# Optimization experiments

Hardware: AMD Instinct MI355X
Metric: run time of the kernel (lower is better)

Reference implementation:

```python
import jax, jax.numpy as jnp
import numpy as np

N, E, IN, H, D, G = 1024, 16384, 1300, 16, 512, 8
SLOPE = 0.2  # PyG GATConv default negative_slope


def gat_conv(x, src, dst, W, a_src, a_dst, b):
    """PyG GATConv (concat heads): per-edge score, segment softmax over dst, scatter-add."""
    n = x.shape[0]
    h = (x @ W).reshape(n, H, D)                       # [N,H,D]
    s_src = jnp.einsum('nhd,hd->nh', h, a_src)         # [N,H]
    s_dst = jnp.einsum('nhd,hd->nh', h, a_dst)
    e = jax.nn.leaky_relu(s_src[src] + s_dst[dst], SLOPE)   # [E,H]
    m = jax.ops.segment_max(e, dst, num_segments=n)
    p = jnp.exp(e - m[dst])
    alpha = p / jax.ops.segment_sum(p, dst, num_segments=n)[dst]
    out = jax.ops.segment_sum(alpha[:, :, None] * h[src], dst, num_segments=n)  # [N,H,D]
    return out.reshape(n, H * D) + b


def setup_inputs() -> dict:
    key = jax.random.key(0)
    ks = jax.random.split(key, 12)
    s = 0.05
    return {
        'x': jax.random.normal(ks[0], (N, IN), jnp.float32),
        'edge_index': jax.random.randint(ks[1], (2, E), 0, N),
        'batch': jnp.sort(jax.random.randint(ks[2], (N,), 0, G)),
        'W1': jax.random.normal(ks[3], (IN, H * D), jnp.float32) * s,
        'att_src1': jax.random.normal(ks[4], (H, D), jnp.float32) * s,
        'att_dst1': jax.random.normal(ks[5], (H, D), jnp.float32) * s,
        'b1': jnp.zeros((H * D,), jnp.float32),
        'W2': jax.random.normal(ks[6], (H * D, H * D), jnp.float32) * s,
        'att_src2': jax.random.normal(ks[7], (H, D), jnp.float32) * s,
        'att_dst2': jax.random.normal(ks[8], (H, D), jnp.float32) * s,
        'b2': jnp.zeros((H * D,), jnp.float32),
        'lin_w': jax.random.normal(ks[9], (H * D, 1), jnp.float32) * s,
        'lin_b': jnp.zeros((1,), jnp.float32),
    }


def reference(x, edge_index, batch, W1, att_src1, att_dst1, b1,
              W2, att_src2, att_dst2, b2, lin_w, lin_b):
    loops = jnp.arange(N, dtype=edge_index.dtype)      # add_self_loops=True
    src = jnp.concatenate([edge_index[0], loops])
    dst = jnp.concatenate([edge_index[1], loops])
    h = jax.nn.relu(gat_conv(x, src, dst, W1, att_src1, att_dst1, b1))
    h = jax.nn.relu(gat_conv(h, src, dst, W2, att_src2, att_dst2, b2))
    counts = jax.ops.segment_sum(jnp.ones((N,), h.dtype), batch, num_segments=G)
    pooled = jax.ops.segment_sum(h, batch, num_segments=G) / jnp.clip(counts, 1.0)[:, None]
    return (pooled @ lin_w + lin_b).squeeze(-1)        # [G]
```

## Files before the change

### kernel.cpp

```cpp
#include <hip/hip_runtime.h>


#define NN      1024
#define EE      16384
#define IN_DIM  1300
#define NH      16
#define HD      512
#define FD      8192
#define NG      8
#define ET      (EE + NN)
#define SLOPE   0.2f

typedef __attribute__((ext_vector_type(8))) short short8;
typedef __attribute__((ext_vector_type(4))) float f32x4;


__global__ void k_init_counts(int* counts) {
    int i = blockIdx.x * 256 + threadIdx.x;
    if (i < NN) counts[i] = 1;
}

__global__ void k_count(const int* __restrict__ dst, int* counts) {
    int e = blockIdx.x * 256 + threadIdx.x;
    if (e < EE) atomicAdd(&counts[dst[e]], 1);
}

__global__ void k_scan(const int* __restrict__ counts, int* __restrict__ off,
                       int* __restrict__ cursor) {
    __shared__ int s[NN];
    int t = threadIdx.x;
    s[t] = counts[t];
    __syncthreads();
    for (int d = 1; d < NN; d <<= 1) {
        int v = (t >= d) ? s[t - d] : 0;
        __syncthreads();
        s[t] += v;
        __syncthreads();
    }
    off[t + 1] = s[t];
    if (t == 0) off[0] = 0;
    cursor[t] = 0;
}

__global__ void k_fill(const int* __restrict__ srcv, const int* __restrict__ dstv,
                       const int* __restrict__ off, int* cursor, int* __restrict__ csr) {
    int e = blockIdx.x * 256 + threadIdx.x;
    if (e < EE) {
        int d = dstv[e];
        int p = atomicAdd(&cursor[d], 1);
        csr[off[d] + p] = srcv[e];
    } else if (e < ET) {
        int n = e - EE;
        int p = atomicAdd(&cursor[n], 1);
        csr[off[n] + p] = n;
    }
}


__device__ __forceinline__ int swz2(int r) {
    return (((r >> 1) & 3) ^ ((r >> 4) & 3)) << 3;
}
__device__ __forceinline__ int swz(int r) {
    return ((r & 3) ^ ((r >> 4) & 3)) << 3;
}

__device__ __forceinline__ unsigned short bf16_rne(float f) {
    unsigned int u = __float_as_uint(f);
    u += 0x7FFF + ((u >> 16) & 1);
    return (unsigned short)(u >> 16);
}

__device__ __forceinline__ void split2(float f, unsigned short& h, unsigned short& l) {
    unsigned short hh = bf16_rne(f);
    float hf = __uint_as_float(((unsigned int)hh) << 16);
    h = hh;
    l = bf16_rne(f - hf);
}


__global__ __launch_bounds__(256) void k_conv_a(const float* __restrict__ S,
                                                unsigned short* __restrict__ H,
                                                unsigned short* __restrict__ L,
                                                int K, int KT) {
    const int chunk = blockIdx.x;
    const int mt = chunk / KT, kt = chunk - mt * KT;
    const int tid = threadIdx.x;
    const size_t ob = (size_t)chunk * 4096;
#pragma unroll
    for (int half = 0; half < 2; half++) {
        const int r = (tid >> 2) + half * 64;
        const int kc0 = (tid & 3) << 3;
        const int k = kt * 32 + (kc0 ^ swz2(r));
        const float* src = S + (size_t)(mt * 128 + r) * K + k;
        float4 f0 = make_float4(0.f, 0.f, 0.f, 0.f), f1 = f0;
        if (k < K)     f0 = *(const float4*)src;
        if (k + 4 < K) f1 = *(const float4*)(src + 4);
        float vals[8] = {f0.x, f0.y, f0.z, f0.w, f1.x, f1.y, f1.z, f1.w};
        short8 hv, lv;
#pragma unroll
        for (int j = 0; j < 8; j++) {
            unsigned short h, l;
            split2(vals[j], h, l);
            hv[j] = (short)h;
            lv[j] = (short)l;
        }
        *(short8*)(H + ob + r * 32 + kc0) = hv;
        *(short8*)(L + ob + r * 32 + kc0) = lv;
    }
}

__global__ __launch_bounds__(256) void k_conv_b(const float* __restrict__ S,
                                                unsigned short* __restrict__ H,
                                                unsigned short* __restrict__ L,
                                                int K, int Nn, int KT) {
    __shared__ float T[128][33];
    const int chunk = blockIdx.x;
    const int nt = chunk / KT, kt = chunk - nt * KT;
    const int tid = threadIdx.x;
    {
        const int kr = tid >> 3;
        const int c0 = (tid & 7) << 4;
        const int k = kt * 32 + kr;
        const float* row = S + (size_t)k * Nn + nt * 128 + c0;
#pragma unroll
        for (int j = 0; j < 4; j++) {
            float4 v = (k < K) ? *(const float4*)(row + (j << 2))
                               : make_float4(0.f, 0.f, 0.f, 0.f);
            T[c0 + (j << 2) + 0][kr] = v.x;
            T[c0 + (j << 2) + 1][kr] = v.y;
            T[c0 + (j << 2) + 2][kr] = v.z;
            T[c0 + (j << 2) + 3][kr] = v.w;
        }
    }
    __syncthreads();
    const size_t ob = (size_t)chunk * 4096;
#pragma unroll
    for (int half = 0; half < 2; half++) {
        const int n = (tid >> 2) + half * 64;
        const int kc0 = (tid & 3) << 3;
        const int ks = kc0 ^ swz2(n);
        short8 hv, lv;
#pragma unroll
        for (int j = 0; j < 8; j++) {
            unsigned short h, l;
            split2(T[n][ks + j], h, l);
            hv[j] = (short)h;
            lv[j] = (short)l;
        }
        *(short8*)(H + ob + n * 32 + kc0) = hv;
        *(short8*)(L + ob + n * 32 + kc0) = lv;
    }
}


__global__ __launch_bounds__(256, 2) void k_gemm_planes(
        const unsigned short* __restrict__ Ahp, const unsigned short* __restrict__ Alp,
        const unsigned short* __restrict__ Bhp, const unsigned short* __restrict__ Blp,
        float* __restrict__ C, int KT, int Nn) {
    __shared__ short smem[4][4096];
    const int tid = threadIdx.x;
    const int lane = tid & 63;
    const int wid = tid >> 6;
    const int wr = wid >> 1, wc = wid & 1;
    const int l15 = lane & 15, l4 = lane >> 4;

    const size_t aoff = (size_t)blockIdx.y * KT * 4096;
    const size_t boff = (size_t)blockIdx.x * KT * 4096;

    f32x4 acc[4][4];
#pragma unroll
    for (int i = 0; i < 4; i++)
#pragma unroll
        for (int j = 0; j < 4; j++) acc[i][j] = (f32x4){0.f, 0.f, 0.f, 0.f};

    short8 st[4][2];
    {
        const size_t ab = aoff + tid * 8, bb = boff + tid * 8;
#pragma unroll
        for (int p = 0; p < 2; p++) {
            st[0][p] = *(const short8*)(Ahp + ab + p * 2048);
            st[1][p] = *(const short8*)(Alp + ab + p * 2048);
            st[2][p] = *(const short8*)(Bhp + bb + p * 2048);
            st[3][p] = *(const short8*)(Blp + bb + p * 2048);
        }
    }

    for (int t = 0; t < KT; t++) {
        __syncthreads();
#pragma unroll
        for (int pl = 0; pl < 4; pl++)
#pragma unroll
            for (int p = 0; p < 2; p++)
                *(short8*)&smem[pl][p * 2048 + tid * 8] = st[pl][p];

        if (t + 1 < KT) {
            const size_t ab = aoff + (size_t)(t + 1) * 4096 + tid * 8;
            const size_t bb = boff + (size_t)(t + 1) * 4096 + tid * 8;
#pragma unroll
            for (int p = 0; p < 2; p++) {
                st[0][p] = *(const short8*)(Ahp + ab + p * 2048);
                st[1][p] = *(const short8*)(Alp + ab + p * 2048);
                st[2][p] = *(const short8*)(Bhp + bb + p * 2048);
                st[3][p] = *(const short8*)(Blp + bb + p * 2048);
            }
        }
        __syncthreads();

        short8 ahf[4], alf[4];
#pragma unroll
        for (int i = 0; i < 4; i++) {
            int m = wr * 64 + i * 16 + l15;
            int ks = (l4 << 3) ^ swz2(m);
            ahf[i] = *(const short8*)&smem[0][m * 32 + ks];
            alf[i] = *(const short8*)&smem[1][m * 32 + ks];
        }
#pragma unroll
        for (int j = 0; j < 4; j++) {
            int n = wc * 64 + j * 16 + l15;
            int ks = (l4 << 3) ^ swz2(n);
            short8 bhf = *(const short8*)&smem[2][n * 32 + ks];
            short8 blf = *(const short8*)&smem[3][n * 32 + ks];
#pragma unroll
            for (int i = 0; i < 4; i++) {
                acc[i][j] = __builtin_amdgcn_mfma_f32_16x16x32_bf16(ahf[i], bhf, acc[i][j], 0, 0, 0);
                acc[i][j] = __builtin_amdgcn_mfma_f32_16x16x32_bf16(ahf[i], blf, acc[i][j], 0, 0, 0);
                acc[i][j] = __builtin_amdgcn_mfma_f32_16x16x32_bf16(alf[i], bhf, acc[i][j], 0, 0, 0);
            }
        }
    }

    float* Cp = C + (size_t)(blockIdx.y * 128 + wr * 64 + (l4 << 2)) * Nn
                  + blockIdx.x * 128 + wc * 64 + l15;
#pragma unroll
    for (int i = 0; i < 4; i++) {
#pragma unroll
        for (int r = 0; r < 4; r++) {
            float* rowp = Cp + (size_t)(i * 16 + r) * Nn;
#pragma unroll
            for (int j = 0; j < 4; j++)
                rowp[j * 16] = acc[i][j][r];
        }
    }
}


__global__ __launch_bounds__(256, 2) void k_gemm_mfma(const float* __restrict__ A,
                                                      const float* __restrict__ B,
                                                      float* __restrict__ C,
                                                      int M, int K, int Nn) {
    __shared__ unsigned short Ah[128][32];
    __shared__ unsigned short Al[128][32];
    __shared__ unsigned short Bh[128][32];
    __shared__ unsigned short Bl[128][32];

    const int tid = threadIdx.x;
    const int lane = tid & 63;
    const int wid = tid >> 6;
    const int wr = wid >> 1, wc = wid & 1;
    const int l15 = lane & 15, l4 = lane >> 4;

    const int a_r  = tid >> 1;
    const int a_k0 = (tid & 1) << 4;
    const int b_k  = tid >> 3;
    const int b_n0 = (tid & 7) << 4;

    const float* Ap = A + (size_t)(blockIdx.y * 128 + a_r) * K;
    const float* Bp = B + (size_t)blockIdx.x * 128 + b_n0;

    f32x4 acc[4][4];
#pragma unroll
    for (int i = 0; i < 4; i++)
#pragma unroll
        for (int j = 0; j < 4; j++) acc[i][j] = (f32x4){0.f, 0.f, 0.f, 0.f};

    const int nt = (K + 31) >> 5;
    const float4 z4 = make_float4(0.f, 0.f, 0.f, 0.f);

    float4 areg[4], breg[4];
    {
#pragma unroll
        for (int j = 0; j < 4; j++) {
            int k = a_k0 + (j << 2);
            areg[j] = (k < K) ? *(const float4*)(Ap + k) : z4;
        }
        bool bok = b_k < K;
#pragma unroll
        for (int j = 0; j < 4; j++)
            breg[j] = bok ? *(const float4*)(Bp + (size_t)b_k * Nn + (j << 2)) : z4;
    }

    for (int t = 0; t < nt; t++) {
        __syncthreads();
#pragma unroll
        for (int j = 0; j < 4; j++) {
            int kk = a_k0 + (j << 2);
            int ks = kk ^ swz(a_r);
            ushort4 h, l;
            split2(areg[j].x, h.x, l.x);
            split2(areg[j].y, h.y, l.y);
            split2(areg[j].z, h.z, l.z);
            split2(areg[j].w, h.w, l.w);
            *(ushort4*)&Ah[a_r][ks] = h;
            *(ushort4*)&Al[a_r][ks] = l;
        }
#pragma unroll
        for (int j = 0; j < 4; j++) {
            const float* bf = (const float*)&breg[j];
#pragma unroll
            for (int c = 0; c < 4; c++) {
                int n = b_n0 + (j << 2) + c;
                unsigned short h, l;
                split2(bf[c], h, l);
                int ks = b_k ^ swz(n);
                Bh[n][ks] = h;
                Bl[n][ks] = l;
            }
        }

        if (t + 1 < nt) {
            const int k0 = (t + 1) << 5;
#pragma unroll
            for (int j = 0; j < 4; j++) {
                int k = k0 + a_k0 + (j << 2);
                areg[j] = (k < K) ? *(const float4*)(Ap + k) : z4;
            }
            bool bok = (k0 + b_k) < K;
#pragma unroll
            for (int j = 0; j < 4; j++)
                breg[j] = bok ? *(const float4*)(Bp + (size_t)(k0 + b_k) * Nn + (j << 2)) : z4;
        }

        __syncthreads();

        short8 ahf[4], alf[4];
#pragma unroll
        for (int i = 0; i < 4; i++) {
            int m = wr * 64 + i * 16 + l15;
            int ks = (l4 << 3) ^ swz(m);
            ahf[i] = *(const short8*)&Ah[m][ks];
            alf[i] = *(const short8*)&Al[m][ks];
        }
#pragma unroll
        for (int j = 0; j < 4; j++) {
            int n = wc * 64 + j * 16 + l15;
            int ks = (l4 << 3) ^ swz(n);
            short8 bhf = *(const short8*)&Bh[n][ks];
            short8 blf = *(const short8*)&Bl[n][ks];
#pragma unroll
            for (int i = 0; i < 4; i++) {
                acc[i][j] = __builtin_amdgcn_mfma_f32_16x16x32_bf16(ahf[i], bhf, acc[i][j], 0, 0, 0);
                acc[i][j] = __builtin_amdgcn_mfma_f32_16x16x32_bf16(ahf[i], blf, acc[i][j], 0, 0, 0);
                acc[i][j] = __builtin_amdgcn_mfma_f32_16x16x32_bf16(alf[i], bhf, acc[i][j], 0, 0, 0);
            }
        }
    }

    float* Cp = C + (size_t)(blockIdx.y * 128 + wr * 64 + (l4 << 2)) * Nn
                  + blockIdx.x * 128 + wc * 64 + l15;
#pragma unroll
    for (int i = 0; i < 4; i++) {
#pragma unroll
        for (int r = 0; r < 4; r++) {
            float* rowp = Cp + (size_t)(i * 16 + r) * Nn;
#pragma unroll
            for (int j = 0; j < 4; j++)
                rowp[j * 16] = acc[i][j][r];
        }
    }
}


__global__ __launch_bounds__(256) void k_scores(const float* __restrict__ h,
                                                const float* __restrict__ a_src,
                                                const float* __restrict__ a_dst,
                                                float* __restrict__ s_src,
                                                float* __restrict__ s_dst) {
    int wid = (blockIdx.x * 256 + threadIdx.x) >> 6;
    int lane = threadIdx.x & 63;
    if (wid >= NN * NH) return;
    int n = wid >> 4, hh = wid & 15;
    const float* hp = h + (size_t)n * FD + hh * HD;
    const float* as = a_src + hh * HD;
    const float* ad = a_dst + hh * HD;
    float ss = 0.f, sd = 0.f;
    for (int d = lane; d < HD; d += 64) {
        float v = hp[d];
        ss += v * as[d];
        sd += v * ad[d];
    }
#pragma unroll
    for (int o = 32; o > 0; o >>= 1) {
        ss += __shfl_xor(ss, o);
        sd += __shfl_xor(sd, o);
    }
    if (lane == 0) { s_src[wid] = ss; s_dst[wid] = sd; }
}


#define MAXCH 64

__global__ __launch_bounds__(256) void k_attn(const float* __restrict__ h,
                                              const float* __restrict__ s_src,
                                              const float* __restrict__ s_dst,
                                              const int* __restrict__ off,
                                              const int* __restrict__ csr,
                                              const float* __restrict__ bias,
                                              float* __restrict__ out) {
    const int t = blockIdx.x;
    const int tid = threadIdx.x;
    __shared__ float m_sh[NH], den_sh[NH];
    __shared__ float alpha[MAXCH][NH];
    __shared__ int src_sh[MAXCH];

    const int e0 = off[t], e1 = off[t + 1];

    if (tid < NH) {
        int hh = tid;
        float sd = s_dst[t * NH + hh];
        float m = -3.0e38f;
        for (int e = e0; e < e1; e++) {
            float v = s_src[csr[e] * NH + hh] + sd;
            v = v > 0.f ? v : SLOPE * v;
            m = fmaxf(m, v);
        }
        float den = 0.f;
        for (int e = e0; e < e1; e++) {
            float v = s_src[csr[e] * NH + hh] + sd;
            v = v > 0.f ? v : SLOPE * v;
            den += __expf(v - m);
        }
        m_sh[hh] = m;
        den_sh[hh] = den;
    }
    __syncthreads();

    float acc[32];
#pragma unroll
    for (int j = 0; j < 32; j++) acc[j] = 0.f;

    for (int c0 = e0; c0 < e1; c0 += MAXCH) {
        int ch = min(MAXCH, e1 - c0);
        for (int i = tid; i < ch * NH; i += 256) {
            int e = i >> 4, hh = i & 15;
            int s = csr[c0 + e];
            if (hh == 0) src_sh[e] = s;
            float v = s_src[s * NH + hh] + s_dst[t * NH + hh];
            v = v > 0.f ? v : SLOPE * v;
            alpha[e][hh] = __expf(v - m_sh[hh]) / den_sh[hh];
        }
        __syncthreads();
        for (int e = 0; e < ch; e++) {
            const float* hp = h + (size_t)src_sh[e] * FD;
#pragma unroll
            for (int j = 0; j < 32; j++)
                acc[j] += alpha[e][j >> 1] * hp[tid + (j << 8)];
        }
        __syncthreads();
    }

#pragma unroll
    for (int j = 0; j < 32; j++) {
        int f = tid + (j << 8);
        float v = acc[j] + bias[f];
        out[(size_t)t * FD + f] = v > 0.f ? v : 0.f;
    }
}


__global__ __launch_bounds__(256) void k_pool(const float* __restrict__ h,
                                              const int* __restrict__ batch,
                                              float* __restrict__ pooled) {
    __shared__ int b_sh[NN];
    const int tid = threadIdx.x;
    const int f = blockIdx.x * 256 + tid;
    for (int i = tid; i < NN; i += 256) b_sh[i] = batch[i];
    __syncthreads();
    float acc[NG];
    int cnt[NG];
#pragma unroll
    for (int g = 0; g < NG; g++) { acc[g] = 0.f; cnt[g] = 0; }
    for (int n = 0; n < NN; n++) {
        int bg = b_sh[n];
        float v = h[(size_t)n * FD + f];
#pragma unroll
        for (int g = 0; g < NG; g++) {
            acc[g] += (bg == g) ? v : 0.f;
            cnt[g] += (bg == g) ? 1 : 0;
        }
    }
#pragma unroll
    for (int g = 0; g < NG; g++)
        pooled[(size_t)g * FD + f] = acc[g] / fmaxf((float)cnt[g], 1.f);
}

__global__ __launch_bounds__(256) void k_final(const float* __restrict__ pooled,
                                               const float* __restrict__ lin_w,
                                               const float* __restrict__ lin_b,
                                               float* __restrict__ outv) {
    const int g = blockIdx.x;
    const int tid = threadIdx.x;
    float s = 0.f;
    for (int f = tid; f < FD; f += 256)
        s += pooled[(size_t)g * FD + f] * lin_w[f];
    __shared__ float red[256];
    red[tid] = s;
    __syncthreads();
    for (int o = 128; o > 0; o >>= 1) {
        if (tid < o) red[tid] += red[tid + o];
        __syncthreads();
    }
    if (tid == 0) outv[g] = red[0] + lin_b[0];
}


extern "C" void kernel_launch(void* const* d_in, const int* in_sizes, int n_in,
                              void* d_out, int out_size, void* d_ws, size_t ws_size,
                              hipStream_t stream) {
    const float* x   = (const float*)d_in[0];
    const int*   ei  = (const int*)d_in[1];
    const int*   bat = (const int*)d_in[2];
    const float* W1  = (const float*)d_in[3];
    const float* as1 = (const float*)d_in[4];
    const float* ad1 = (const float*)d_in[5];
    const float* b1  = (const float*)d_in[6];
    const float* W2  = (const float*)d_in[7];
    const float* as2 = (const float*)d_in[8];
    const float* ad2 = (const float*)d_in[9];
    const float* b2  = (const float*)d_in[10];
    const float* lw  = (const float*)d_in[11];
    const float* lb  = (const float*)d_in[12];

    char* p0 = (char*)d_ws;
    char* p = p0;
    auto alloc = [&](size_t bytes) {
        char* r = p;
        p += (bytes + 255) & ~size_t(255);
        return r;
    };
    int* counts   = (int*)alloc((NN + 1) * sizeof(int));
    int* off      = (int*)alloc((NN + 1) * sizeof(int));
    int* cursor   = (int*)alloc(NN * sizeof(int));
    int* csr      = (int*)alloc(ET * sizeof(int));
    float* ssrc   = (float*)alloc((size_t)NN * NH * sizeof(float));
    float* sdst   = (float*)alloc((size_t)NN * NH * sizeof(float));
    float* hbuf   = (float*)alloc((size_t)NN * FD * sizeof(float));
    float* abuf   = (float*)alloc((size_t)NN * FD * sizeof(float));
    float* pooled = (float*)alloc((size_t)NG * FD * sizeof(float));

    const int KT1 = (IN_DIM + 31) / 32;
    const int KT2 = FD / 32;
    const size_t sz_xp  = (size_t)(NN / 128) * KT1 * 4096;
    const size_t sz_w1p = (size_t)(FD / 128) * KT1 * 4096;
    const size_t sz_w2p = (size_t)(FD / 128) * KT2 * 4096;
    const size_t sz_h2p = (size_t)(NN / 128) * KT2 * 4096;
    unsigned short* xH  = (unsigned short*)alloc(sz_xp * 2);
    unsigned short* xL  = (unsigned short*)alloc(sz_xp * 2);
    unsigned short* w1H = (unsigned short*)alloc(sz_w1p * 2);
    unsigned short* w1L = (unsigned short*)alloc(sz_w1p * 2);
    unsigned short* w2H = (unsigned short*)alloc(sz_w2p * 2);
    unsigned short* w2L = (unsigned short*)alloc(sz_w2p * 2);
    unsigned short* h2H = (unsigned short*)alloc(sz_h2p * 2);
    unsigned short* h2L = (unsigned short*)alloc(sz_h2p * 2);
    const bool planes_ok = (size_t)(p - p0) <= ws_size;

    const int* esrc = ei;
    const int* edst = ei + EE;

    k_init_counts<<<(NN + 255) / 256, 256, 0, stream>>>(counts);
    k_count<<<(EE + 255) / 256, 256, 0, stream>>>(edst, counts);
    k_scan<<<1, NN, 0, stream>>>(counts, off, cursor);
    k_fill<<<(ET + 255) / 256, 256, 0, stream>>>(esrc, edst, off, cursor, csr);

    dim3 gg(FD / 128, NN / 128);

    if (planes_ok) {
        k_conv_a<<<(NN / 128) * KT1, 256, 0, stream>>>(x, xH, xL, IN_DIM, KT1);
        k_conv_b<<<(FD / 128) * KT1, 256, 0, stream>>>(W1, w1H, w1L, IN_DIM, FD, KT1);
        k_conv_b<<<(FD / 128) * KT2, 256, 0, stream>>>(W2, w2H, w2L, FD, FD, KT2);
        k_gemm_planes<<<gg, 256, 0, stream>>>(xH, xL, w1H, w1L, hbuf, KT1, FD);
    } else {
        k_gemm_mfma<<<gg, 256, 0, stream>>>(x, W1, hbuf, NN, IN_DIM, FD);
    }
    k_scores<<<NN * NH / 4, 256, 0, stream>>>(hbuf, as1, ad1, ssrc, sdst);
    k_attn<<<NN, 256, 0, stream>>>(hbuf, ssrc, sdst, off, csr, b1, abuf);

    if (planes_ok) {
        k_conv_a<<<(NN / 128) * KT2, 256, 0, stream>>>(abuf, h2H, h2L, FD, KT2);
        k_gemm_planes<<<gg, 256, 0, stream>>>(h2H, h2L, w2H, w2L, hbuf, KT2, FD);
    } else {
        k_gemm_mfma<<<gg, 256, 0, stream>>>(abuf, W2, hbuf, NN, FD, FD);
    }
    k_scores<<<NN * NH / 4, 256, 0, stream>>>(hbuf, as2, ad2, ssrc, sdst);
    k_attn<<<NN, 256, 0, stream>>>(hbuf, ssrc, sdst, off, csr, b2, abuf);

    k_pool<<<FD / 256, 256, 0, stream>>>(abuf, bat, pooled);
    k_final<<<NG, 256, 0, stream>>>(pooled, lw, lb, (float*)d_out);
}
```

Before: 1.394 ms.

## Recast sparse attention aggregation as dense per-head attention-matrix GEMM

Replaces the gather-based k_attn aggregation with a dense path. Softmax stats are computed per destination node, the normalized edge weights are scattered into a dense [H,N,N] matrix, and that matrix is split into bf16 hi/lo planes. A per-head GEMM against the transposed h planes then does the aggregation, with bias and ReLU fused into its epilogue. The planes GEMM also switches to double-buffered direct global-to-LDS loads. The cost is a 64MB matrix that must be zeroed and converted, doing dense work on a graph with about 1.6% density.

```diff
diff --git a/kernel.cpp b/kernel.cpp
--- a/kernel.cpp
+++ b/kernel.cpp
@@ -42,6 +42,23 @@
     cursor[t] = 0;
 }
 
+__global__ void k_fill2(const int* __restrict__ srcv, const int* __restrict__ dstv,
+                        const int* __restrict__ off, int* cursor,
+                        int* __restrict__ csr, int* __restrict__ csr_dst) {
+    int e = blockIdx.x * 256 + threadIdx.x;
+    if (e < EE) {
+        int d = dstv[e];
+        int p = atomicAdd(&cursor[d], 1);
+        csr[off[d] + p] = srcv[e];
+        csr_dst[off[d] + p] = d;
+    } else if (e < ET) {
+        int n = e - EE;
+        int p = atomicAdd(&cursor[n], 1);
+        csr[off[n] + p] = n;
+        csr_dst[off[n] + p] = n;
+    }
+}
+
 __global__ void k_fill(const int* __restrict__ srcv, const int* __restrict__ dstv,
                        const int* __restrict__ off, int* cursor, int* __restrict__ csr) {
     int e = blockIdx.x * 256 + threadIdx.x;
@@ -75,6 +92,12 @@
     float hf = __uint_as_float(((unsigned int)hh) << 16);
     h = hh;
     l = bf16_rne(f - hf);
+}
+
+__device__ __forceinline__ void gload16(const void* g, void* l) {
+    __builtin_amdgcn_global_load_lds((const __attribute__((address_space(1))) void*)g,
+                                     (__attribute__((address_space(3))) void*)l,
+                                     16, 0, 0);
 }
 
 
@@ -152,19 +175,111 @@
     }
 }
 
+__global__ __launch_bounds__(256) void k_conv_pa(const float* __restrict__ Pf,
+                                                 unsigned short* __restrict__ H,
+                                                 unsigned short* __restrict__ L) {
+    const int chunk = blockIdx.x;
+    const int head = chunk >> 8;
+    const int rem = chunk & 255;
+    const int mt = rem >> 5, kt = rem & 31;
+    const int tid = threadIdx.x;
+    const size_t ob = (size_t)chunk * 4096;
+    const float* base = Pf + (size_t)head * NN * NN;
+#pragma unroll
+    for (int half = 0; half < 2; half++) {
+        const int r = (tid >> 2) + half * 64;
+        const int kc0 = (tid & 3) << 3;
+        const int k = kt * 32 + (kc0 ^ swz2(r));
+        const float* src = base + (size_t)(mt * 128 + r) * NN + k;
+        float4 f0 = *(const float4*)src;
+        float4 f1 = *(const float4*)(src + 4);
+        float vals[8] = {f0.x, f0.y, f0.z, f0.w, f1.x, f1.y, f1.z, f1.w};
+        short8 hv, lv;
+#pragma unroll
+        for (int j = 0; j < 8; j++) {
+            unsigned short h, l;
+            split2(vals[j], h, l);
+            hv[j] = (short)h;
+            lv[j] = (short)l;
+        }
+        *(short8*)(H + ob + r * 32 + kc0) = hv;
+        *(short8*)(L + ob + r * 32 + kc0) = lv;
+    }
+}
+
+
+__global__ __launch_bounds__(256) void k_stats(const float* __restrict__ ssrc,
+                                               const float* __restrict__ sdstv,
+                                               const int* __restrict__ off,
+                                               const int* __restrict__ csr,
+                                               float* __restrict__ md,
+                                               float* __restrict__ dn) {
+    const int t = blockIdx.x;
+    const int i = threadIdx.x;
+    const int head = i >> 4, sub = i & 15;
+    const int e0 = off[t], e1 = off[t + 1];
+    const float sd = sdstv[t * NH + head];
+    float m = -3.0e38f;
+    for (int e = e0 + sub; e < e1; e += 16) {
+        float v = ssrc[csr[e] * NH + head] + sd;
+        v = v > 0.f ? v : SLOPE * v;
+        m = fmaxf(m, v);
+    }
+#pragma unroll
+    for (int o = 8; o > 0; o >>= 1) m = fmaxf(m, __shfl_xor(m, o));
+    float den = 0.f;
+    for (int e = e0 + sub; e < e1; e += 16) {
+        float v = ssrc[csr[e] * NH + head] + sd;
+        v = v > 0.f ? v : SLOPE * v;
+        den += __expf(v - m);
+    }
+#pragma unroll
+    for (int o = 8; o > 0; o >>= 1) den += __shfl_xor(den, o);
+    if (sub == 0) { md[t * NH + head] = m; dn[t * NH + head] = den; }
+}
+
+__global__ void k_zero4(float4* __restrict__ p, int n4) {
+    int i = blockIdx.x * 256 + threadIdx.x;
+    const int stride = gridDim.x * 256;
+    const float4 z = make_float4(0.f, 0.f, 0.f, 0.f);
+    for (; i < n4; i += stride) p[i] = z;
+}
+
+__global__ __launch_bounds__(256) void k_scatter(const int* __restrict__ csr,
+                                                 const int* __restrict__ csr_dst,
+                                                 const float* __restrict__ ssrc,
+                                                 const float* __restrict__ sdstv,
+                                                 const float* __restrict__ md,
+                                                 const float* __restrict__ dn,
+                                                 float* __restrict__ Pf) {
+    const int e = blockIdx.x * 256 + threadIdx.x;
+    if (e >= ET) return;
+    const int s = csr[e], t = csr_dst[e];
+#pragma unroll
+    for (int hh = 0; hh < NH; hh++) {
+        float v = ssrc[s * NH + hh] + sdstv[t * NH + hh];
+        v = v > 0.f ? v : SLOPE * v;
+        float a = __expf(v - md[t * NH + hh]) / dn[t * NH + hh];
+        atomicAdd(&Pf[(size_t)hh * NN * NN + (size_t)t * NN + s], a);
+    }
+}
+
 
 __global__ __launch_bounds__(256, 2) void k_gemm_planes(
         const unsigned short* __restrict__ Ahp, const unsigned short* __restrict__ Alp,
         const unsigned short* __restrict__ Bhp, const unsigned short* __restrict__ Blp,
-        float* __restrict__ C, int KT, int Nn) {
-    __shared__ short smem[4][4096];
+        float* __restrict__ C, int KT, int Nn,
+        const float* __restrict__ bias, int relu, int headed) {
+    __shared__ short smem[2][4][4096];
     const int tid = threadIdx.x;
     const int lane = tid & 63;
     const int wid = tid >> 6;
     const int wr = wid >> 1, wc = wid & 1;
     const int l15 = lane & 15, l4 = lane >> 4;
 
-    const size_t aoff = (size_t)blockIdx.y * KT * 4096;
+    const size_t amt = headed ? ((size_t)(blockIdx.x >> 2) * 8 + blockIdx.y)
+                              : (size_t)blockIdx.y;
+    const size_t aoff = amt * KT * 4096;
     const size_t boff = (size_t)blockIdx.x * KT * 4096;
 
     f32x4 acc[4][4];
@@ -173,53 +288,45 @@
 #pragma unroll
         for (int j = 0; j < 4; j++) acc[i][j] = (f32x4){0.f, 0.f, 0.f, 0.f};
 
-    short8 st[4][2];
-    {
-        const size_t ab = aoff + tid * 8, bb = boff + tid * 8;
-#pragma unroll
-        for (int p = 0; p < 2; p++) {
-            st[0][p] = *(const short8*)(Ahp + ab + p * 2048);
-            st[1][p] = *(const short8*)(Alp + ab + p * 2048);
-            st[2][p] = *(const short8*)(Bhp + bb + p * 2048);
-            st[3][p] = *(const short8*)(Blp + bb + p * 2048);
-        }
-    }
-
-    for (int t = 0; t < KT; t++) {
-        __syncthreads();
-#pragma unroll
-        for (int pl = 0; pl < 4; pl++)
-#pragma unroll
-            for (int p = 0; p < 2; p++)
-                *(short8*)&smem[pl][p * 2048 + tid * 8] = st[pl][p];
-
-        if (t + 1 < KT) {
-            const size_t ab = aoff + (size_t)(t + 1) * 4096 + tid * 8;
-            const size_t bb = boff + (size_t)(t + 1) * 4096 + tid * 8;
-#pragma unroll
-            for (int p = 0; p < 2; p++) {
-                st[0][p] = *(const short8*)(Ahp + ab + p * 2048);
-                st[1][p] = *(const short8*)(Alp + ab + p * 2048);
-                st[2][p] = *(const short8*)(Bhp + bb + p * 2048);
-                st[3][p] = *(const short8*)(Blp + bb + p * 2048);
-            }
-        }
-        __syncthreads();
-
+    const int thg = (wid << 9) + (lane << 3);
+    const int ldw = (wid << 9);
+
+    auto STAGE = [&](int b, int t2) {
+        const size_t ca = aoff + (size_t)t2 * 4096;
+        const size_t cb = boff + (size_t)t2 * 4096;
+#pragma unroll
+        for (int q = 0; q < 2; q++) {
+            const int so = (q << 11) + thg;
+            const int lo = (q << 11) + ldw;
+            gload16(Ahp + ca + so, &smem[b][0][lo]);
+            gload16(Alp + ca + so, &smem[b][1][lo]);
+            gload16(Bhp + cb + so, &smem[b][2][lo]);
+            gload16(Blp + cb + so, &smem[b][3][lo]);
+        }
+    };
+
+    STAGE(0, 0);
+    STAGE(1, 1);
+    asm volatile("s_waitcnt vmcnt(8)" ::: "memory");
+    __builtin_amdgcn_sched_barrier(0);
+    __builtin_amdgcn_s_barrier();
+
+    int cur = 0;
+    for (int t = 0; t < KT; ++t) {
         short8 ahf[4], alf[4];
 #pragma unroll
         for (int i = 0; i < 4; i++) {
             int m = wr * 64 + i * 16 + l15;
             int ks = (l4 << 3) ^ swz2(m);
-            ahf[i] = *(const short8*)&smem[0][m * 32 + ks];
-            alf[i] = *(const short8*)&smem[1][m * 32 + ks];
+            ahf[i] = *(const short8*)&smem[cur][0][m * 32 + ks];
+            alf[i] = *(const short8*)&smem[cur][1][m * 32 + ks];
         }
 #pragma unroll
         for (int j = 0; j < 4; j++) {
             int n = wc * 64 + j * 16 + l15;
             int ks = (l4 << 3) ^ swz2(n);
-            short8 bhf = *(const short8*)&smem[2][n * 32 + ks];
-            short8 blf = *(const short8*)&smem[3][n * 32 + ks];
+            short8 bhf = *(const short8*)&smem[cur][2][n * 32 + ks];
+            short8 blf = *(const short8*)&smem[cur][3][n * 32 + ks];
 #pragma unroll
             for (int i = 0; i < 4; i++) {
                 acc[i][j] = __builtin_amdgcn_mfma_f32_16x16x32_bf16(ahf[i], bhf, acc[i][j], 0, 0, 0);
@@ -227,18 +334,41 @@
                 acc[i][j] = __builtin_amdgcn_mfma_f32_16x16x32_bf16(alf[i], bhf, acc[i][j], 0, 0, 0);
             }
         }
-    }
-
-    float* Cp = C + (size_t)(blockIdx.y * 128 + wr * 64 + (l4 << 2)) * Nn
-                  + blockIdx.x * 128 + wc * 64 + l15;
+
+        if (t + 1 < KT) {
+            asm volatile("s_waitcnt lgkmcnt(0)" ::: "memory");
+            __builtin_amdgcn_sched_barrier(0);
+            __builtin_amdgcn_s_barrier();
+            __builtin_amdgcn_sched_barrier(0);
+            if (t + 2 < KT) {
+                STAGE(cur, t + 2);
+                asm volatile("s_waitcnt vmcnt(8)" ::: "memory");
+            } else {
+                asm volatile("s_waitcnt vmcnt(0)" ::: "memory");
+            }
+            __builtin_amdgcn_sched_barrier(0);
+            __builtin_amdgcn_s_barrier();
+            cur ^= 1;
+        }
+    }
+
+    const int col0 = blockIdx.x * 128 + wc * 64 + l15;
+    float bj[4];
+#pragma unroll
+    for (int j = 0; j < 4; j++) bj[j] = bias ? bias[col0 + j * 16] : 0.f;
+
+    float* Cp = C + (size_t)(blockIdx.y * 128 + wr * 64 + (l4 << 2)) * Nn + col0;
 #pragma unroll
     for (int i = 0; i < 4; i++) {
 #pragma unroll
         for (int r = 0; r < 4; r++) {
             float* rowp = Cp + (size_t)(i * 16 + r) * Nn;
 #pragma unroll
-            for (int j = 0; j < 4; j++)
-                rowp[j * 16] = acc[i][j][r];
+            for (int j = 0; j < 4; j++) {
+                float v = acc[i][j][r] + bj[j];
+                if (relu) v = fmaxf(v, 0.f);
+                rowp[j * 16] = v;
+            }
         }
     }
 }
@@ -563,35 +693,75 @@
     unsigned short* h2L = (unsigned short*)alloc(sz_h2p * 2);
     const bool planes_ok = (size_t)(p - p0) <= ws_size;
 
+    const size_t sz_pp = (size_t)NH * 256 * 4096;
+    const size_t sz_hb = (size_t)(FD / 128) * 32 * 4096;
+    int*   csr_dst = (int*)alloc(ET * sizeof(int));
+    float* md      = (float*)alloc((size_t)NN * NH * sizeof(float));
+    float* dn      = (float*)alloc((size_t)NN * NH * sizeof(float));
+    unsigned short* PpH = (unsigned short*)alloc(sz_pp * 2);
+    unsigned short* PpL = (unsigned short*)alloc(sz_pp * 2);
+    char* U = alloc((size_t)NH * NN * NN * sizeof(float));
+    float* Pf = (float*)U;
+    unsigned short* HbH = (unsigned short*)U;
+    unsigned short* HbL = HbH + sz_hb;
+    const bool attn_ok = planes_ok && (size_t)(p - p0) <= ws_size;
+
     const int* esrc = ei;
     const int* edst = ei + EE;
 
     k_init_counts<<<(NN + 255) / 256, 256, 0, stream>>>(counts);
     k_count<<<(EE + 255) / 256, 256, 0, stream>>>(edst, counts);
     k_scan<<<1, NN, 0, stream>>>(counts, off, cursor);
-    k_fill<<<(ET + 255) / 256, 256, 0, stream>>>(esrc, edst, off, cursor, csr);
+    if (attn_ok)
+        k_fill2<<<(ET + 255) / 256, 256, 0, stream>>>(esrc, edst, off, cursor, csr, csr_dst);
+    else
+        k_fill<<<(ET + 255) / 256, 256, 0, stream>>>(esrc, edst, off, cursor, csr);
 
     dim3 gg(FD / 128, NN / 128);
+    dim3 ga(FD / 128, NN / 128);
+    const int nzero4 = NH * NN * NN / 4;
 
     if (planes_ok) {
         k_conv_a<<<(NN / 128) * KT1, 256, 0, stream>>>(x, xH, xL, IN_DIM, KT1);
         k_conv_b<<<(FD / 128) * KT1, 256, 0, stream>>>(W1, w1H, w1L, IN_DIM, FD, KT1);
         k_conv_b<<<(FD / 128) * KT2, 256, 0, stream>>>(W2, w2H, w2L, FD, FD, KT2);
-        k_gemm_planes<<<gg, 256, 0, stream>>>(xH, xL, w1H, w1L, hbuf, KT1, FD);
+        k_gemm_planes<<<gg, 256, 0, stream>>>(xH, xL, w1H, w1L, hbuf, KT1, FD,
+                                              nullptr, 0, 0);
     } else {
         k_gemm_mfma<<<gg, 256, 0, stream>>>(x, W1, hbuf, NN, IN_DIM, FD);
     }
     k_scores<<<NN * NH / 4, 256, 0, stream>>>(hbuf, as1, ad1, ssrc, sdst);
-    k_attn<<<NN, 256, 0, stream>>>(hbuf, ssrc, sdst, off, csr, b1, abuf);
+    if (attn_ok) {
+        k_stats<<<NN, 256, 0, stream>>>(ssrc, sdst, off, csr, md, dn);
+        k_zero4<<<2048, 256, 0, stream>>>((float4*)Pf, nzero4);
+        k_scatter<<<(ET + 255) / 256, 256, 0, stream>>>(csr, csr_dst, ssrc, sdst, md, dn, Pf);
+        k_conv_pa<<<NH * 256, 256, 0, stream>>>(Pf, PpH, PpL);
+        k_conv_b<<<(FD / 128) * 32, 256, 0, stream>>>(hbuf, HbH, HbL, NN, FD, 32);
+        k_gemm_planes<<<ga, 256, 0, stream>>>(PpH, PpL, HbH, HbL, abuf, 32, FD,
+                                              b1, 1, 1);
+    } else {
+        k_attn<<<NN, 256, 0, stream>>>(hbuf, ssrc, sdst, off, csr, b1, abuf);
+    }
 
     if (planes_ok) {
         k_conv_a<<<(NN / 128) * KT2, 256, 0, stream>>>(abuf, h2H, h2L, FD, KT2);
-        k_gemm_planes<<<gg, 256, 0, stream>>>(h2H, h2L, w2H, w2L, hbuf, KT2, FD);
+        k_gemm_planes<<<gg, 256, 0, stream>>>(h2H, h2L, w2H, w2L, hbuf, KT2, FD,
+                                              nullptr, 0, 0);
     } else {
         k_gemm_mfma<<<gg, 256, 0, stream>>>(abuf, W2, hbuf, NN, FD, FD);
     }
     k_scores<<<NN * NH / 4, 256, 0, stream>>>(hbuf, as2, ad2, ssrc, sdst);
-    k_attn<<<NN, 256, 0, stream>>>(hbuf, ssrc, sdst, off, csr, b2, abuf);
+    if (attn_ok) {
+        k_stats<<<NN, 256, 0, stream>>>(ssrc, sdst, off, csr, md, dn);
+        k_zero4<<<2048, 256, 0, stream>>>((float4*)Pf, nzero4);
+        k_scatter<<<(ET + 255) / 256, 256, 0, stream>>>(csr, csr_dst, ssrc, sdst, md, dn, Pf);
+        k_conv_pa<<<NH * 256, 256, 0, stream>>>(Pf, PpH, PpL);
+        k_conv_b<<<(FD / 128) * 32, 256, 0, stream>>>(hbuf, HbH, HbL, NN, FD, 32);
+        k_gemm_planes<<<ga, 256, 0, stream>>>(PpH, PpL, HbH, HbL, abuf, 32, FD,
+                                              b2, 1, 1);
+    } else {
+        k_attn<<<NN, 256, 0, stream>>>(hbuf, ssrc, sdst, off, csr, b2, abuf);
+    }
 
     k_pool<<<FD / 256, 256, 0, stream>>>(abuf, bat, pooled);
     k_final<<<NG, 256, 0, stream>>>(pooled, lw, lb, (float*)d_out);
```

Measured after the change: 1.377 ms. No clear change (-1.3%).
